# Performance work log

Measured on AMD Instinct MI355X. Metric: run time of the kernel, lower is better.

The kernel has to match this reference:

```python
import jax, jax.numpy as jnp
import numpy as np

N_QUBITS = 8
TRASH = 1
DEPTH = 2
DIM = 2 ** N_QUBITS  # 256

# Qiskit little-endian: amplitude index k has qubit 0 as LSB. Reshaping a
# 256-vector to (2,)*8 puts qubit (N-1-a) on tensor axis a (axis 0 = MSB).
# Observable j is SparsePauliOp with 'Z' at string pos j => Z on qubit N-1-j
# => tensor axis j. So exp_j = sum probs * (1 - 2*bit_axis_j).


def _rx(t):
    c = jnp.cos(t / 2).astype(jnp.complex64)
    ms = (-1j * jnp.sin(t / 2)).astype(jnp.complex64)
    return jnp.stack([jnp.stack([c, ms]), jnp.stack([ms, c])])


def _ry(t):
    c = jnp.cos(t / 2).astype(jnp.complex64)
    s = jnp.sin(t / 2).astype(jnp.complex64)
    return jnp.stack([jnp.stack([c, -s]), jnp.stack([s, c])])


def _rz(t):
    e = jnp.exp((-0.5j) * t.astype(jnp.complex64))
    z = jnp.zeros_like(e)
    return jnp.stack([jnp.stack([e, z]), jnp.stack([z, jnp.conj(e)])])


def _apply_1q(psi, U, q):
    ax = 1 + (N_QUBITS - 1 - q)
    return jnp.moveaxis(jnp.tensordot(psi, U, axes=([ax], [1])), -1, ax)


def _apply_cx(psi, c, t):
    axc = 1 + (N_QUBITS - 1 - c)
    axt = 1 + (N_QUBITS - 1 - t)
    shape = [1] * psi.ndim
    shape[axc] = 2
    ctrl = (jnp.arange(2).reshape(shape) == 1)
    return jnp.where(ctrl, jnp.flip(psi, axis=axt), psi)


def _r3_ansatz(psi, theta, nq, depth):
    k = 0
    for _ in range(depth):
        for q in range(nq):
            psi = _apply_1q(psi, _rx(theta[k + 0]), q)
            psi = _apply_1q(psi, _ry(theta[k + 1]), q)
            psi = _apply_1q(psi, _rz(theta[k + 2]), q)
            k += 3
        for q in range(nq - 1):  # linear entanglement
            psi = _apply_cx(psi, q, q + 1)
    return psi


# sign matrix for Z expectations: S[j, k] = 1 - 2*bit_{N-1-j}(k)
_k = np.arange(DIM)
_SIGNS = np.stack([1.0 - 2.0 * ((_k >> (N_QUBITS - 1 - j)) & 1)
                   for j in range(N_QUBITS)]).astype(np.float32)  # (8, 256)


def setup_inputs() -> dict:
    key = jax.random.key(0)
    k1, k2, k3, k4 = jax.random.split(key, 4)
    return {
        "x": jax.random.normal(k1, (32, 1024, 256), dtype=jnp.float32),
        "theta1": jax.random.normal(k2, (DEPTH * N_QUBITS * 3,), dtype=jnp.float32),
        "theta2": jax.random.normal(k3, (DEPTH * (N_QUBITS - TRASH) * 3,), dtype=jnp.float32),
        "theta3": jax.random.normal(k4, (DEPTH * N_QUBITS * 3,), dtype=jnp.float32),
    }


def reference(x, theta1, theta2, theta3):
    B, T, D = x.shape
    xf = x.reshape(B * T, D)
    # amplitude encode: normalize classical vector into quantum amplitudes
    norm = jnp.linalg.norm(xf, axis=1, keepdims=True)
    norm = jnp.where(norm == 0, jnp.float32(1e-8), norm)
    psi = (xf / norm).astype(jnp.complex64).reshape((B * T,) + (2,) * N_QUBITS)
    # ansatz: U1 (8q) -> U2 (7q) -> U3 (8q)
    psi = _r3_ansatz(psi, theta1, N_QUBITS, DEPTH)
    psi = _r3_ansatz(psi, theta2, N_QUBITS - TRASH, DEPTH)
    psi = _r3_ansatz(psi, theta3, N_QUBITS, DEPTH)
    # Z expectation on each observable
    probs = (jnp.abs(psi) ** 2).reshape(B * T, DIM)
    y = probs @ jnp.asarray(_SIGNS).T  # (B*T, 8)
    # amplitude decode: normalize, |.|^2, zero-pad to DIM
    yn = jnp.linalg.norm(y, axis=1, keepdims=True)
    yn = jnp.where(yn == 0, jnp.float32(1e-8), yn)
    cv = (y / yn) ** 2
    out = jnp.pad(cv, ((0, 0), (0, DIM - N_QUBITS)))
    return out.reshape(B, T, DIM)
```

## Files before the change

kernel.cpp:

```cpp
#include <hip/hip_runtime.h>
#include <math.h>


#define DEV __device__ __forceinline__

typedef __attribute__((ext_vector_type(8))) _Float16 half8;
typedef __attribute__((ext_vector_type(4))) float f32x4;

DEV float2 cmul(float2 a, float2 b) {
  return make_float2(a.x * b.x - a.y * b.y, a.x * b.y + a.y * b.x);
}
DEV float2 cadd(float2 a, float2 b) { return make_float2(a.x + b.x, a.y + b.y); }

DEV unsigned short f16b(float v) {
  _Float16 h = (_Float16)v;
  return __builtin_bit_cast(unsigned short, h);
}

template <int CTRL>
DEV float dppf(float v) {
  return __int_as_float(__builtin_amdgcn_mov_dpp(__float_as_int(v), CTRL, 0xF, 0xF, true));
}
DEV float px1(float v) { return dppf<0xB1>(v); }
DEV float px2(float v) { return dppf<0x4E>(v); }
DEV float px4(float v) { return dppf<0x1B>(dppf<0x141>(v)); }
DEV float px8(float v) { return dppf<0x141>(dppf<0x140>(v)); }
DEV float fsgn(float v, int m) { return __int_as_float(__float_as_int(v) ^ m); }


struct Psi4 { float re[4]; float im[4]; };

template <int Q>
DEV void pair_gate(Psi4& s, const float2* __restrict__ Mlo,
                   const float2* __restrict__ Mhi, int lane) {
  const int b0 = (lane >> Q) & 1, b1 = (lane >> (Q + 1)) & 1;
  float2 lo_d = Mlo[b0 * 2 + b0];
  float2 lo_o = Mlo[b0 * 2 + (b0 ^ 1)];
  float2 hi_d = Mhi[b1 * 2 + b1];
  float2 hi_o = Mhi[b1 * 2 + (b1 ^ 1)];
  float2 c00 = cmul(hi_d, lo_d);
  float2 c01 = cmul(hi_d, lo_o);
  float2 c10 = cmul(hi_o, lo_d);
  float2 c11 = cmul(hi_o, lo_o);
  const int m0 = 1 << Q, m1 = 2 << Q;
#pragma unroll
  for (int r = 0; r < 4; ++r) {
    float ar = s.re[r], ai = s.im[r];
    float p0r = __shfl_xor(ar, m0, 64), p0i = __shfl_xor(ai, m0, 64);
    float p1r = __shfl_xor(ar, m1, 64), p1i = __shfl_xor(ai, m1, 64);
    float p2r = __shfl_xor(ar, m0 | m1, 64), p2i = __shfl_xor(ai, m0 | m1, 64);
    float nr = c00.x * ar - c00.y * ai + c01.x * p0r - c01.y * p0i
             + c10.x * p1r - c10.y * p1i + c11.x * p2r - c11.y * p2i;
    float ni = c00.x * ai + c00.y * ar + c01.x * p0i + c01.y * p0r
             + c10.x * p1i + c10.y * p1r + c11.x * p2i + c11.y * p2r;
    s.re[r] = nr; s.im[r] = ni;
  }
}

DEV void regpair_gate(Psi4& s, const float2* __restrict__ Mlo,
                      const float2* __restrict__ Mhi) {
  float nr[4], ni[4];
#pragma unroll
  for (int r = 0; r < 4; ++r) {
    const int b0 = r & 1, b1 = (r >> 1) & 1;
    float2 c00 = cmul(Mhi[b1 * 2 + b1], Mlo[b0 * 2 + b0]);
    float2 c01 = cmul(Mhi[b1 * 2 + b1], Mlo[b0 * 2 + (b0 ^ 1)]);
    float2 c10 = cmul(Mhi[b1 * 2 + (b1 ^ 1)], Mlo[b0 * 2 + b0]);
    float2 c11 = cmul(Mhi[b1 * 2 + (b1 ^ 1)], Mlo[b0 * 2 + (b0 ^ 1)]);
    nr[r] = c00.x * s.re[r] - c00.y * s.im[r]
          + c01.x * s.re[r ^ 1] - c01.y * s.im[r ^ 1]
          + c10.x * s.re[r ^ 2] - c10.y * s.im[r ^ 2]
          + c11.x * s.re[r ^ 3] - c11.y * s.im[r ^ 3];
    ni[r] = c00.x * s.im[r] + c00.y * s.re[r]
          + c01.x * s.im[r ^ 1] + c01.y * s.re[r ^ 1]
          + c10.x * s.im[r ^ 2] + c10.y * s.re[r ^ 2]
          + c11.x * s.im[r ^ 3] + c11.y * s.re[r ^ 3];
  }
#pragma unroll
  for (int r = 0; r < 4; ++r) { s.re[r] = nr[r]; s.im[r] = ni[r]; }
}

DEV void reg0_gate(Psi4& s, const float2* __restrict__ M) {
  float nr[4], ni[4];
#pragma unroll
  for (int r = 0; r < 4; ++r) {
    const int b = r & 1;
    float2 d = M[b * 2 + b], o = M[b * 2 + (b ^ 1)];
    nr[r] = d.x * s.re[r] - d.y * s.im[r] + o.x * s.re[r ^ 1] - o.y * s.im[r ^ 1];
    ni[r] = d.x * s.im[r] + d.y * s.re[r] + o.x * s.im[r ^ 1] + o.y * s.re[r ^ 1];
  }
#pragma unroll
  for (int r = 0; r < 4; ++r) { s.re[r] = nr[r]; s.im[r] = ni[r]; }
}

template <bool FULL8>
DEV void perm_cx(Psi4& s, int lane) {
  const int slane = (lane ^ (lane << 1)) & 63;
  const bool L5 = ((lane >> 5) & 1) != 0;
  float nr[4], ni[4];
#pragma unroll
  for (int r = 0; r < 4; ++r) {
    const int r0 = r & 1, r1 = (r >> 1) & 1;
    const int hiBit = FULL8 ? (r1 ^ r0) : r1;
    const int sA = (hiBit << 1) | r0;
    const int sB = sA ^ 1;
    float aRe = __shfl(s.re[sA], slane, 64);
    float aIm = __shfl(s.im[sA], slane, 64);
    float bRe = __shfl(s.re[sB], slane, 64);
    float bIm = __shfl(s.im[sB], slane, 64);
    nr[r] = L5 ? bRe : aRe;
    ni[r] = L5 ? bIm : aIm;
  }
#pragma unroll
  for (int r = 0; r < 4; ++r) { s.re[r] = nr[r]; s.im[r] = ni[r]; }
}

template <int NQ>
DEV void ansatz_f(Psi4& s, const float2* __restrict__ Mg, int lane) {
#pragma unroll
  for (int d = 0; d < 2; ++d) {
    const float2* Md = Mg + d * NQ * 4;
    pair_gate<0>(s, Md + 0, Md + 4, lane);
    pair_gate<2>(s, Md + 8, Md + 12, lane);
    pair_gate<4>(s, Md + 16, Md + 20, lane);
    if (NQ == 8) regpair_gate(s, Md + 24, Md + 28);
    else reg0_gate(s, Md + 24);
    perm_cx<NQ == 8>(s, lane);
  }
}

DEV void store_v(unsigned short* __restrict__ Vsw, int n, int kk, float v) {
  int k = kk >> 5, rem = kk & 31, quad = rem >> 3, jj = rem & 7;
  int nn = n & 255;
  int w = (nn >> 6) & 3, t = (nn >> 4) & 3, cl = nn & 15;
  int g = w * 8 + ((n >= 256) ? 4 + t : t);
  int L = quad * 16 + cl;
  size_t base = (size_t)k * 16384 + (size_t)g * 512 + (size_t)L * 8 + jj;
  Vsw[base] = f16b(v);
}

__global__ void build_u(const float* __restrict__ th1, const float* __restrict__ th2,
                        const float* __restrict__ th3, unsigned short* __restrict__ Vsw) {
  __shared__ float2 Mg[46 * 4];
  const int tid = threadIdx.x;
  if (tid < 46) {
    float thx, thy, thz;
    if (tid < 16)      { thx = th1[tid * 3]; thy = th1[tid * 3 + 1]; thz = th1[tid * 3 + 2]; }
    else if (tid < 30) { int u = (tid - 16) * 3; thx = th2[u]; thy = th2[u + 1]; thz = th2[u + 2]; }
    else               { int u = (tid - 30) * 3; thx = th3[u]; thy = th3[u + 1]; thz = th3[u + 2]; }
    float sx, cx_, sy, cy_, sz, cz_;
    sincosf(0.5f * thx, &sx, &cx_);
    sincosf(0.5f * thy, &sy, &cy_);
    sincosf(0.5f * thz, &sz, &cz_);
    float2 rx[4] = {{cx_, 0}, {0, -sx}, {0, -sx}, {cx_, 0}};
    float2 ry[4] = {{cy_, 0}, {-sy, 0}, {sy, 0}, {cy_, 0}};
    float2 A0 = cadd(cmul(ry[0], rx[0]), cmul(ry[1], rx[2]));
    float2 A1 = cadd(cmul(ry[0], rx[1]), cmul(ry[1], rx[3]));
    float2 A2 = cadd(cmul(ry[2], rx[0]), cmul(ry[3], rx[2]));
    float2 A3 = cadd(cmul(ry[2], rx[1]), cmul(ry[3], rx[3]));
    float2 ezm = make_float2(cz_, -sz), ezp = make_float2(cz_, sz);
    Mg[tid * 4 + 0] = cmul(ezm, A0);
    Mg[tid * 4 + 1] = cmul(ezm, A1);
    Mg[tid * 4 + 2] = cmul(ezp, A2);
    Mg[tid * 4 + 3] = cmul(ezp, A3);
  }
  __syncthreads();

  const int lane = tid & 63;
  const int j = blockIdx.x * 4 + (tid >> 6);
  Psi4 s;
#pragma unroll
  for (int r = 0; r < 4; ++r) {
    int a = (r << 6) | lane;
    s.re[r] = (a == j) ? 1.f : 0.f;
    s.im[r] = 0.f;
  }
  ansatz_f<8>(s, Mg, lane);
  ansatz_f<7>(s, Mg + 16 * 4, lane);
  ansatz_f<8>(s, Mg + 30 * 4, lane);
#pragma unroll
  for (int r = 0; r < 4; ++r) {
    int a = (r << 6) | lane;
    store_v(Vsw, a, j, s.re[r]);
    store_v(Vsw, a + 256, j, s.im[r]);
  }
}


__global__ __launch_bounds__(512, 4) void pqc_main(const float* __restrict__ x,
                                                   const unsigned short* __restrict__ Vsw,
                                                   float* __restrict__ out) {
  const int tid = threadIdx.x;
  const int ww = tid >> 6;
  const int w = ww >> 1;
  const int half = ww & 1;
  const int L = tid & 63;
  const int quad = L >> 4;
  const int c = L & 15;
  const int row0 = blockIdx.x * 64;

  __shared__ unsigned short A2[8][4][512];
  __shared__ float ys[64][8];
  __shared__ float invn[64];
  float* part = (float*)&A2[0][0][0];

  const unsigned short* pb = Vsw + (size_t)w * 4096 + (size_t)half * 2048 + (size_t)L * 8;

  half8 b0 = *(const half8*)(pb);
  half8 b1 = *(const half8*)(pb + 512);

  {
    const float4* xsrc = (const float4*)(x + (size_t)row0 * 256);
    const int r8 = L & 7;
    const int kf = L >> 3;
    const int q = kf >> 1;
    const int jj0 = (kf & 1) * 4;
#pragma unroll
    for (int i = 0; i < 8; ++i) {
      int row = i * 8 + r8;
      float4 f = xsrc[row * 64 + ww * 8 + kf];
      ushort4 h;
      h.x = f16b(f.x); h.y = f16b(f.y); h.z = f16b(f.z); h.w = f16b(f.w);
      int mt = row >> 4, cc = row & 15;
      int idx = (q * 16 + (cc ^ (q << 1))) * 8 + jj0;
      *(ushort4*)&A2[ww][mt][idx] = h;
    }
  }
  __syncthreads();

  f32x4 acc[4][4];
#pragma unroll
  for (int mt = 0; mt < 4; ++mt)
#pragma unroll
    for (int tt = 0; tt < 4; ++tt) acc[mt][tt] = (f32x4){0.f, 0.f, 0.f, 0.f};

  const int sL8 = (quad * 16 + (c ^ (quad << 1))) * 8;

#pragma unroll 1
  for (int k = 0; k < 8; ++k) {
    half8 ah[4];
#pragma unroll
    for (int mt = 0; mt < 4; ++mt)
      ah[mt] = *(const half8*)&A2[k][mt][sL8];
    const unsigned short* pk = pb + (size_t)k * 16384;
    const unsigned short* pn = pb + (size_t)((k < 7) ? k + 1 : k) * 16384;

    half8 b2 = *(const half8*)(pk + 2 * 512);
#pragma unroll
    for (int mt = 0; mt < 4; ++mt)
      acc[mt][0] = __builtin_amdgcn_mfma_f32_16x16x32_f16(ah[mt], b0, acc[mt][0], 0, 0, 0);
    half8 b3 = *(const half8*)(pk + 3 * 512);
#pragma unroll
    for (int mt = 0; mt < 4; ++mt)
      acc[mt][1] = __builtin_amdgcn_mfma_f32_16x16x32_f16(ah[mt], b1, acc[mt][1], 0, 0, 0);
    b0 = *(const half8*)(pn);
#pragma unroll
    for (int mt = 0; mt < 4; ++mt)
      acc[mt][2] = __builtin_amdgcn_mfma_f32_16x16x32_f16(ah[mt], b2, acc[mt][2], 0, 0, 0);
    b1 = *(const half8*)(pn + 512);
#pragma unroll
    for (int mt = 0; mt < 4; ++mt)
      acc[mt][3] = __builtin_amdgcn_mfma_f32_16x16x32_f16(ah[mt], b3, acc[mt][3], 0, 0, 0);
  }
  __syncthreads();

  const int m1 = (c & 1) << 31;
  const int m2 = (c & 2) << 30;
  const int m4 = (c & 4) << 29;
  const int m8 = (c & 8) << 28;
#pragma unroll
  for (int mt = 0; mt < 4; ++mt) {
#pragma unroll
    for (int r = 0; r < 4; ++r) {
      float p0 = acc[mt][0][r] * acc[mt][0][r];
      float p1 = acc[mt][1][r] * acc[mt][1][r];
      float p2 = acc[mt][2][r] * acc[mt][2][r];
      float p3 = acc[mt][3][r] * acc[mt][3][r];
      float s01 = p0 + p1, s23 = p2 + p3;
      float av = s01 + s23;
      float bv = s01 - s23;
      float cv = (p0 - p1) + (p2 - p3);
      av = px1(av) + fsgn(av, m1);
      bv += px1(bv);  cv += px1(cv);
      av = px2(av) + fsgn(av, m2);
      bv += px2(bv);  cv += px2(cv);
      av = px4(av) + fsgn(av, m4);
      bv += px4(bv);  cv += px4(cv);
      av = px8(av) + fsgn(av, m8);
      bv += px8(bv);  cv += px8(cv);
      int m = mt * 16 + quad * 4 + r;
      float* pm = part + (ww * 64 + m) * 8;
      if (c == 0) {
        pm[0] = ((w >> 1) & 1) ? -av : av;
        pm[1] = (w & 1) ? -av : av;
        pm[2] = bv;
        pm[3] = cv;
      } else if (c == 8) pm[4] = av;
      else if (c == 4) pm[5] = av;
      else if (c == 2) pm[6] = av;
      else if (c == 1) pm[7] = av;
    }
  }
  __syncthreads();

  {
    int m = tid >> 3, jj = tid & 7;
    float acc_y = 0.f;
#pragma unroll
    for (int p = 0; p < 8; ++p) acc_y += part[(p * 64 + m) * 8 + jj];
    ys[m][jj] = acc_y;
    float sq = acc_y * acc_y;
    sq += px1(sq);
    sq += px2(sq);
    sq += px4(sq);
    if (jj == 0) invn[m] = (sq == 0.f) ? 0.f : 1.f / sqrtf(sq);
  }
  __syncthreads();

  float4* o4 = (float4*)(out + (size_t)row0 * 256);
#pragma unroll
  for (int i = 0; i < 8; ++i) {
    int e = i * 512 + tid;
    int row = e >> 6;
    int c4 = (e & 63) * 4;
    float4 v = make_float4(0.f, 0.f, 0.f, 0.f);
    if (c4 < 8) {
      float iv = invn[row];
      float t0 = ys[row][c4 + 0] * iv;
      float t1 = ys[row][c4 + 1] * iv;
      float t2 = ys[row][c4 + 2] * iv;
      float t3 = ys[row][c4 + 3] * iv;
      v = make_float4(t0 * t0, t1 * t1, t2 * t2, t3 * t3);
    }
    o4[e] = v;
  }
}

extern "C" void kernel_launch(void* const* d_in, const int* in_sizes, int n_in,
                              void* d_out, int out_size, void* d_ws, size_t ws_size,
                              hipStream_t stream) {
  const float* x = (const float*)d_in[0];
  const float* th1 = (const float*)d_in[1];
  const float* th2 = (const float*)d_in[2];
  const float* th3 = (const float*)d_in[3];
  float* out = (float*)d_out;
  unsigned short* Vsw = (unsigned short*)d_ws;

  build_u<<<64, 256, 0, stream>>>(th1, th2, th3, Vsw);
  pqc_main<<<512, 512, 0, stream>>>(x, Vsw, out);
}
```

Baseline: 108.8 us.

## Retile main GEMM to 32-row blocks of 4 waves owning full column slices

New measurement: 109.1 us. About the same (+0.3%).

```diff
diff --git a/kernel.cpp b/kernel.cpp
--- a/kernel.cpp
+++ b/kernel.cpp
@@ -187,27 +187,20 @@
 }
 
 
-__global__ __launch_bounds__(512, 4) void pqc_main(const float* __restrict__ x,
+__global__ __launch_bounds__(256, 4) void pqc_main(const float* __restrict__ x,
                                                    const unsigned short* __restrict__ Vsw,
                                                    float* __restrict__ out) {
   const int tid = threadIdx.x;
-  const int ww = tid >> 6;
-  const int w = ww >> 1;
-  const int half = ww & 1;
+  const int w = tid >> 6;
   const int L = tid & 63;
   const int quad = L >> 4;
   const int c = L & 15;
-  const int row0 = blockIdx.x * 64;
-
-  __shared__ unsigned short A2[8][4][512];
-  __shared__ float ys[64][8];
-  __shared__ float invn[64];
+  const int row0 = blockIdx.x * 32;
+
+  __shared__ unsigned short A2[8][2][512];
+  __shared__ float ys[32][8];
+  __shared__ float invn[32];
   float* part = (float*)&A2[0][0][0];
-
-  const unsigned short* pb = Vsw + (size_t)w * 4096 + (size_t)half * 2048 + (size_t)L * 8;
-
-  half8 b0 = *(const half8*)(pb);
-  half8 b1 = *(const half8*)(pb + 512);
 
   {
     const float4* xsrc = (const float4*)(x + (size_t)row0 * 256);
@@ -216,51 +209,42 @@
     const int q = kf >> 1;
     const int jj0 = (kf & 1) * 4;
 #pragma unroll
-    for (int i = 0; i < 8; ++i) {
-      int row = i * 8 + r8;
-      float4 f = xsrc[row * 64 + ww * 8 + kf];
-      ushort4 h;
-      h.x = f16b(f.x); h.y = f16b(f.y); h.z = f16b(f.z); h.w = f16b(f.w);
-      int mt = row >> 4, cc = row & 15;
-      int idx = (q * 16 + (cc ^ (q << 1))) * 8 + jj0;
-      *(ushort4*)&A2[ww][mt][idx] = h;
+    for (int ch2 = 0; ch2 < 2; ++ch2) {
+      const int ch = w + ch2 * 4;
+#pragma unroll
+      for (int i = 0; i < 4; ++i) {
+        int row = i * 8 + r8;
+        float4 f = xsrc[row * 64 + ch * 8 + kf];
+        ushort4 h;
+        h.x = f16b(f.x); h.y = f16b(f.y); h.z = f16b(f.z); h.w = f16b(f.w);
+        int mt = row >> 4, cc = row & 15;
+        int idx = (q * 16 + (cc ^ (q << 1))) * 8 + jj0;
+        *(ushort4*)&A2[ch][mt][idx] = h;
+      }
     }
   }
   __syncthreads();
 
-  f32x4 acc[4][4];
-#pragma unroll
-  for (int mt = 0; mt < 4; ++mt)
-#pragma unroll
-    for (int tt = 0; tt < 4; ++tt) acc[mt][tt] = (f32x4){0.f, 0.f, 0.f, 0.f};
-
+  f32x4 acc[2][8];
+#pragma unroll
+  for (int mt = 0; mt < 2; ++mt)
+#pragma unroll
+    for (int tt = 0; tt < 8; ++tt) acc[mt][tt] = (f32x4){0.f, 0.f, 0.f, 0.f};
+
+  const unsigned short* pb = Vsw + (size_t)w * 4096 + (size_t)L * 8;
   const int sL8 = (quad * 16 + (c ^ (quad << 1))) * 8;
 
 #pragma unroll 1
   for (int k = 0; k < 8; ++k) {
-    half8 ah[4];
-#pragma unroll
-    for (int mt = 0; mt < 4; ++mt)
-      ah[mt] = *(const half8*)&A2[k][mt][sL8];
+    half8 ah0 = *(const half8*)&A2[k][0][sL8];
+    half8 ah1 = *(const half8*)&A2[k][1][sL8];
     const unsigned short* pk = pb + (size_t)k * 16384;
-    const unsigned short* pn = pb + (size_t)((k < 7) ? k + 1 : k) * 16384;
-
-    half8 b2 = *(const half8*)(pk + 2 * 512);
-#pragma unroll
-    for (int mt = 0; mt < 4; ++mt)
-      acc[mt][0] = __builtin_amdgcn_mfma_f32_16x16x32_f16(ah[mt], b0, acc[mt][0], 0, 0, 0);
-    half8 b3 = *(const half8*)(pk + 3 * 512);
-#pragma unroll
-    for (int mt = 0; mt < 4; ++mt)
-      acc[mt][1] = __builtin_amdgcn_mfma_f32_16x16x32_f16(ah[mt], b1, acc[mt][1], 0, 0, 0);
-    b0 = *(const half8*)(pn);
-#pragma unroll
-    for (int mt = 0; mt < 4; ++mt)
-      acc[mt][2] = __builtin_amdgcn_mfma_f32_16x16x32_f16(ah[mt], b2, acc[mt][2], 0, 0, 0);
-    b1 = *(const half8*)(pn + 512);
-#pragma unroll
-    for (int mt = 0; mt < 4; ++mt)
-      acc[mt][3] = __builtin_amdgcn_mfma_f32_16x16x32_f16(ah[mt], b3, acc[mt][3], 0, 0, 0);
+#pragma unroll
+    for (int tt = 0; tt < 8; ++tt) {
+      half8 bh = *(const half8*)(pk + tt * 512);
+      acc[0][tt] = __builtin_amdgcn_mfma_f32_16x16x32_f16(ah0, bh, acc[0][tt], 0, 0, 0);
+      acc[1][tt] = __builtin_amdgcn_mfma_f32_16x16x32_f16(ah1, bh, acc[1][tt], 0, 0, 0);
+    }
   }
   __syncthreads();
 
@@ -269,13 +253,13 @@
   const int m4 = (c & 4) << 29;
   const int m8 = (c & 8) << 28;
 #pragma unroll
-  for (int mt = 0; mt < 4; ++mt) {
+  for (int mt = 0; mt < 2; ++mt) {
 #pragma unroll
     for (int r = 0; r < 4; ++r) {
-      float p0 = acc[mt][0][r] * acc[mt][0][r];
-      float p1 = acc[mt][1][r] * acc[mt][1][r];
-      float p2 = acc[mt][2][r] * acc[mt][2][r];
-      float p3 = acc[mt][3][r] * acc[mt][3][r];
+      float p0 = acc[mt][0][r] * acc[mt][0][r] + acc[mt][4][r] * acc[mt][4][r];
+      float p1 = acc[mt][1][r] * acc[mt][1][r] + acc[mt][5][r] * acc[mt][5][r];
+      float p2 = acc[mt][2][r] * acc[mt][2][r] + acc[mt][6][r] * acc[mt][6][r];
+      float p3 = acc[mt][3][r] * acc[mt][3][r] + acc[mt][7][r] * acc[mt][7][r];
       float s01 = p0 + p1, s23 = p2 + p3;
       float av = s01 + s23;
       float bv = s01 - s23;
@@ -289,7 +273,7 @@
       av = px8(av) + fsgn(av, m8);
       bv += px8(bv);  cv += px8(cv);
       int m = mt * 16 + quad * 4 + r;
-      float* pm = part + (ww * 64 + m) * 8;
+      float* pm = part + (w * 32 + m) * 8;
       if (c == 0) {
         pm[0] = ((w >> 1) & 1) ? -av : av;
         pm[1] = (w & 1) ? -av : av;
@@ -305,9 +289,8 @@
 
   {
     int m = tid >> 3, jj = tid & 7;
-    float acc_y = 0.f;
-#pragma unroll
-    for (int p = 0; p < 8; ++p) acc_y += part[(p * 64 + m) * 8 + jj];
+    float acc_y = part[(0 * 32 + m) * 8 + jj] + part[(1 * 32 + m) * 8 + jj]
+                + part[(2 * 32 + m) * 8 + jj] + part[(3 * 32 + m) * 8 + jj];
     ys[m][jj] = acc_y;
     float sq = acc_y * acc_y;
     sq += px1(sq);
@@ -320,7 +303,7 @@
   float4* o4 = (float4*)(out + (size_t)row0 * 256);
 #pragma unroll
   for (int i = 0; i < 8; ++i) {
-    int e = i * 512 + tid;
+    int e = i * 256 + tid;
     int row = e >> 6;
     int c4 = (e & 63) * 4;
     float4 v = make_float4(0.f, 0.f, 0.f, 0.f);
@@ -347,5 +330,5 @@
   unsigned short* Vsw = (unsigned short*)d_ws;
 
   build_u<<<64, 256, 0, stream>>>(th1, th2, th3, Vsw);
-  pqc_main<<<512, 512, 0, stream>>>(x, Vsw, out);
-}
+  pqc_main<<<1024, 256, 0, stream>>>(x, Vsw, out);
+}
```

## Move output zero-fill into setup kernel and write only nonzero outputs in main

Applied to the files above, without the earlier changes.

Measured after the change: 109.1 us. No clear change (+0.2%).

```diff
diff --git a/kernel.cpp b/kernel.cpp
--- a/kernel.cpp
+++ b/kernel.cpp
@@ -140,7 +140,15 @@
 }
 
 __global__ void build_u(const float* __restrict__ th1, const float* __restrict__ th2,
-                        const float* __restrict__ th3, unsigned short* __restrict__ Vsw) {
+                        const float* __restrict__ th3, unsigned short* __restrict__ Vsw,
+                        float4* __restrict__ ofill) {
+  if (blockIdx.x >= 64) {
+    size_t i = (size_t)(blockIdx.x - 64) * 256 + threadIdx.x;
+    float4 z = make_float4(0.f, 0.f, 0.f, 0.f);
+#pragma unroll
+    for (int r = 0; r < 4; ++r) ofill[i + (size_t)r * 524288] = z;
+    return;
+  }
   __shared__ float2 Mg[46 * 4];
   const int tid = threadIdx.x;
   if (tid < 46) {
@@ -200,8 +208,6 @@
   const int row0 = blockIdx.x * 64;
 
   __shared__ unsigned short A2[8][4][512];
-  __shared__ float ys[64][8];
-  __shared__ float invn[64];
   float* part = (float*)&A2[0][0][0];
 
   const unsigned short* pb = Vsw + (size_t)w * 4096 + (size_t)half * 2048 + (size_t)L * 8;
@@ -308,31 +314,13 @@
     float acc_y = 0.f;
 #pragma unroll
     for (int p = 0; p < 8; ++p) acc_y += part[(p * 64 + m) * 8 + jj];
-    ys[m][jj] = acc_y;
     float sq = acc_y * acc_y;
     sq += px1(sq);
     sq += px2(sq);
     sq += px4(sq);
-    if (jj == 0) invn[m] = (sq == 0.f) ? 0.f : 1.f / sqrtf(sq);
-  }
-  __syncthreads();
-
-  float4* o4 = (float4*)(out + (size_t)row0 * 256);
-#pragma unroll
-  for (int i = 0; i < 8; ++i) {
-    int e = i * 512 + tid;
-    int row = e >> 6;
-    int c4 = (e & 63) * 4;
-    float4 v = make_float4(0.f, 0.f, 0.f, 0.f);
-    if (c4 < 8) {
-      float iv = invn[row];
-      float t0 = ys[row][c4 + 0] * iv;
-      float t1 = ys[row][c4 + 1] * iv;
-      float t2 = ys[row][c4 + 2] * iv;
-      float t3 = ys[row][c4 + 3] * iv;
-      v = make_float4(t0 * t0, t1 * t1, t2 * t2, t3 * t3);
-    }
-    o4[e] = v;
+    float iv = (sq == 0.f) ? 0.f : 1.f / sqrtf(sq);
+    float t = acc_y * iv;
+    out[(size_t)(row0 + m) * 256 + jj] = t * t;
   }
 }
 
@@ -346,6 +334,6 @@
   float* out = (float*)d_out;
   unsigned short* Vsw = (unsigned short*)d_ws;
 
-  build_u<<<64, 256, 0, stream>>>(th1, th2, th3, Vsw);
+  build_u<<<2112, 256, 0, stream>>>(th1, th2, th3, Vsw, (float4*)out);
   pqc_main<<<512, 512, 0, stream>>>(x, Vsw, out);
 }
```
